# Optimization experiments

Hardware: AMD Instinct MI355X
Metric: run time of the kernel (lower is better)

The kernel has to match this reference:

```python
import jax, jax.numpy as jnp
import numpy as np


def setup_inputs() -> dict:
    key = jax.random.key(0)
    kq, kk, kv = jax.random.split(key, 3)
    d_head, sq, skv = 128, 8192, 8192
    q = jax.random.normal(kq, (d_head, sq), dtype=jnp.float32)
    k = jax.random.normal(kk, (d_head, skv), dtype=jnp.float32)
    v = jax.random.normal(kv, (d_head, skv), dtype=jnp.float32)
    return {"q": q, "k": k, "v": v}


def reference(q, k, v):
    # qk: (seqlen_q, seqlen_kv) -- full score matrix, no 1/sqrt(d) scaling (faithful)
    qk = jnp.einsum('dq,dk->qk', q, k)
    row_max = jnp.max(qk, axis=1, keepdims=True)
    exp_row = jnp.exp(qk - row_max)
    scores = exp_row / jnp.sum(exp_row, axis=1, keepdims=True)
    # attn_out: (seqlen_q, d_head)
    attn_out = jnp.einsum('qk,dk->qd', scores, v)
    return attn_out
```

## Files before the change

kernel.cpp:

```cpp
#include <hip/hip_runtime.h>
#include <hip/hip_bf16.h>
#include <math.h>

typedef _Float16 half8 __attribute__((ext_vector_type(8)));
typedef __fp16 fp16x2 __attribute__((ext_vector_type(2)));
typedef float f32x4 __attribute__((ext_vector_type(4)));
typedef float f32x16 __attribute__((ext_vector_type(16)));

#define D 128
#define SQ 8192
#define SKV 8192
#define BQ 128
#define BKV 64
#define LOG2E 1.4426950408889634f
#define DEFER_THR 11.5417f

__device__ __forceinline__ ushort f2bf(float x) {
  union { float f; unsigned u; } v; v.f = x;
  unsigned r = v.u + 0x7fffu + ((v.u >> 16) & 1u);
  return (ushort)(r >> 16);
}
__device__ __forceinline__ float bf2f(ushort h) {
  union { unsigned u; float f; } v; v.u = ((unsigned)h) << 16;
  return v.f;
}
__device__ __forceinline__ unsigned cvtpk_bf(float a, float b) {
  unsigned r;
  asm("v_cvt_pk_bf16_f32 %0, %1, %2" : "=v"(r) : "v"(a), "v"(b));
  return r;
}
__device__ __forceinline__ unsigned cvtpk_h(float a, float b) {
  union { fp16x2 h; unsigned u; } r;
  r.h = __builtin_amdgcn_cvt_pkrtz(a, b);
  return r.u;
}
__device__ __forceinline__ float fexp2(float x) {
  float r;
  asm("v_exp_f32 %0, %1" : "=v"(r) : "v"(x));
  return r;
}
__device__ __forceinline__ void pl32swap(unsigned& a, unsigned& b) {
  asm("v_permlane32_swap_b32 %0, %1" : "+v"(a), "+v"(b));
}

__global__ void prep_all(const float* __restrict__ q, const float* __restrict__ k,
                         const float* __restrict__ v,
                         _Float16* __restrict__ QT, _Float16* __restrict__ PK,
                         _Float16* __restrict__ PV) {
  int b = blockIdx.x;
  int t = threadIdx.x;
  if (b < 512) {
    const bool isQ = (b < 256);
    const float* src = isQ ? q : k;
    const float scl = isQ ? LOG2E : 1.0f;
    int s0 = (isQ ? b : b - 256) * 32;
    __shared__ float lds[128][33];
    int dr = t >> 5, l = t & 31;
#pragma unroll
    for (int j = 0; j < 16; ++j) {
      int dd = dr * 16 + j;
      lds[dd][l] = src[(size_t)dd * SQ + s0 + l];
    }
    __syncthreads();
#pragma unroll
    for (int i = 0; i < 2; ++i) {
      int cid = t + i * 256;
      int c = cid >> 5, sl = cid & 31;
      half8 hv;
#pragma unroll
      for (int e = 0; e < 8; ++e) hv[e] = (_Float16)(lds[c * 8 + e][sl] * scl);
      if (isQ) {
        *(half8*)(QT + (size_t)(s0 + sl) * D + c * 8) = hv;
      } else {
        int srow = s0 + sl;
        size_t elem = (size_t)((srow >> 5) * 8 + (c >> 1)) * 512 +
                      ((c & 1) * 32 + (srow & 31)) * 8;
        *(half8*)(PK + elem) = hv;
      }
    }
  } else {
    int idx = (b - 512) * 256 + t;
    int i8 = idx * 8;
    float4 x0 = *(const float4*)(v + i8);
    float4 x1 = *(const float4*)(v + i8 + 4);
    int drow = i8 >> 13;
    int kv = i8 & (SKV - 1);
    size_t elem = (size_t)(kv >> 6) * 8192 +
                  (size_t)((drow >> 5) * 4 + ((kv >> 4) & 3)) * 512 +
                  (((kv >> 3) & 1) * 32 + (drow & 31)) * 8;
    half8 hv = { (_Float16)x0.x, (_Float16)x0.y, (_Float16)x0.z, (_Float16)x0.w,
                 (_Float16)x1.x, (_Float16)x1.y, (_Float16)x1.z, (_Float16)x1.w };
    *(half8*)(PV + elem) = hv;
  }
}

__global__ __launch_bounds__(256, 2)
void flash_fwd(const _Float16* __restrict__ QT, const _Float16* __restrict__ PK,
               const _Float16* __restrict__ PV,
               ushort* __restrict__ Opart, float* __restrict__ Mst,
               float* __restrict__ Lst, int splitLen) {
  __shared__ _Float16 Kl[2][BKV * D];
  __shared__ _Float16 Vl[2][BKV * D];

  if (blockIdx.y & 4) __builtin_amdgcn_s_sleep(60);

  const int tid = threadIdx.x;
  const int w = tid >> 6;
  const int lane = tid & 63;
  const int lc = lane & 31;
  const int hi = lane >> 5;
  const int qb = blockIdx.x;
  const int split = blockIdx.y;
  const int qrow = qb * BQ + w * 32 + lc;

  half8 qh[8];
#pragma unroll
  for (int ds = 0; ds < 8; ++ds)
    qh[ds] = *(const half8*)(QT + (size_t)qrow * D + ds * 16 + hi * 8);

  f32x16 Ot[4];
#pragma unroll
  for (int dt = 0; dt < 4; ++dt)
#pragma unroll
    for (int e = 0; e < 16; ++e) Ot[dt][e] = 0.f;
  float mrun = -INFINITY, lrun = 0.f;

  const int kvBase = split * splitLen;
  const int nsteps = splitLen / BKV;

#define STAGE(NB, KV0)                                                        \
  {                                                                           \
    _Pragma("unroll")                                                         \
    for (int j = 0; j < 8; ++j) {                                             \
      int cblk = w * 8 + j;                                                   \
      int cc = cblk & 15;                                                     \
      const _Float16* gp = ((cblk < 16) ? PK : PV) +                          \
                           (size_t)(KV0) * D + cc * 512 + lane * 8;           \
      _Float16* lp = ((cblk < 16) ? &Kl[NB][0] : &Vl[NB][0]) + cc * 512;      \
      __builtin_amdgcn_global_load_lds(                                       \
          (const __attribute__((address_space(1))) unsigned*)gp,              \
          (__attribute__((address_space(3))) unsigned*)lp, 16, 0, 0);         \
    }                                                                         \
  }

  STAGE(0, kvBase);
  __syncthreads();
  int cur = 0;

  for (int it = 0; it < nsteps; ++it) {
    const int kv0 = kvBase + it * BKV;
    const bool more = (it + 1 < nsteps);
    if (more) STAGE(cur ^ 1, kv0 + BKV);

    const _Float16* kb = &Kl[cur][0] + lane * 8;
    const _Float16* vb = &Vl[cur][0] + lane * 8;

    half8 ka[16];
#pragma unroll
    for (int j = 0; j < 16; ++j) ka[j] = *(const half8*)(kb + j * 512);

    f32x16 s0, s1;
#pragma unroll
    for (int e = 0; e < 16; ++e) { s0[e] = 0.f; s1[e] = 0.f; }
    __builtin_amdgcn_s_setprio(1);
#pragma unroll
    for (int ds = 0; ds < 8; ++ds) {
      s0 = __builtin_amdgcn_mfma_f32_32x32x16_f16(ka[ds], qh[ds], s0, 0, 0, 0);
      s1 = __builtin_amdgcn_mfma_f32_32x32x16_f16(ka[8 + ds], qh[ds], s1, 0, 0, 0);
    }
    __builtin_amdgcn_s_setprio(0);

    half8 va[16];
#pragma unroll
    for (int f = 0; f < 16; ++f) va[f] = *(const half8*)(vb + f * 512);

    float t8[8];
#pragma unroll
    for (int e = 0; e < 8; ++e)
      t8[e] = fmaxf(fmaxf(s0[e], s0[e + 8]), fmaxf(s1[e], s1[e + 8]));
    float mx = fmaxf(fmaxf(fmaxf(t8[0], t8[4]), fmaxf(t8[1], t8[5])),
                     fmaxf(fmaxf(t8[2], t8[6]), fmaxf(t8[3], t8[7])));
    mx = fmaxf(mx, __shfl_xor(mx, 32));

    if (!__all(mx - mrun <= DEFER_THR)) {
      float mn = fmaxf(mrun, mx);
      float sc = fexp2(mrun - mn);
      mrun = mn;
      lrun *= sc;
#pragma unroll
      for (int dt = 0; dt < 4; ++dt)
#pragma unroll
        for (int e = 0; e < 16; ++e) Ot[dt][e] *= sc;
    }

#pragma unroll
    for (int e = 0; e < 16; ++e) {
      s0[e] = fexp2(s0[e] - mrun);
      s1[e] = fexp2(s1[e] - mrun);
    }
    float a8[8];
#pragma unroll
    for (int e = 0; e < 8; ++e) a8[e] = (s0[e] + s0[e + 8]) + (s1[e] + s1[e + 8]);
    float lsum = ((a8[0] + a8[4]) + (a8[1] + a8[5])) +
                 ((a8[2] + a8[6]) + (a8[3] + a8[7]));
    lsum += __shfl_xor(lsum, 32);
    lrun += lsum;

    unsigned pk[8];
    half8 pb[4];
    union { unsigned u[4]; half8 v; } pbu;
#pragma unroll
    for (int j = 0; j < 8; ++j) pk[j] = cvtpk_h(s0[2 * j], s0[2 * j + 1]);
    pl32swap(pk[0], pk[2]); pl32swap(pk[1], pk[3]);
    pl32swap(pk[4], pk[6]); pl32swap(pk[5], pk[7]);
    pbu.u[0] = pk[0]; pbu.u[1] = pk[1]; pbu.u[2] = pk[2]; pbu.u[3] = pk[3]; pb[0] = pbu.v;
    pbu.u[0] = pk[4]; pbu.u[1] = pk[5]; pbu.u[2] = pk[6]; pbu.u[3] = pk[7]; pb[1] = pbu.v;
#pragma unroll
    for (int j = 0; j < 8; ++j) pk[j] = cvtpk_h(s1[2 * j], s1[2 * j + 1]);
    pl32swap(pk[0], pk[2]); pl32swap(pk[1], pk[3]);
    pl32swap(pk[4], pk[6]); pl32swap(pk[5], pk[7]);
    pbu.u[0] = pk[0]; pbu.u[1] = pk[1]; pbu.u[2] = pk[2]; pbu.u[3] = pk[3]; pb[2] = pbu.v;
    pbu.u[0] = pk[4]; pbu.u[1] = pk[5]; pbu.u[2] = pk[6]; pbu.u[3] = pk[7]; pb[3] = pbu.v;

    __builtin_amdgcn_s_setprio(1);
#pragma unroll
    for (int cc = 0; cc < 4; ++cc) {
      Ot[0] = __builtin_amdgcn_mfma_f32_32x32x16_f16(va[0 * 4 + cc], pb[cc], Ot[0], 0, 0, 0);
      Ot[1] = __builtin_amdgcn_mfma_f32_32x32x16_f16(va[1 * 4 + cc], pb[cc], Ot[1], 0, 0, 0);
      Ot[2] = __builtin_amdgcn_mfma_f32_32x32x16_f16(va[2 * 4 + cc], pb[cc], Ot[2], 0, 0, 0);
      Ot[3] = __builtin_amdgcn_mfma_f32_32x32x16_f16(va[3 * 4 + cc], pb[cc], Ot[3], 0, 0, 0);
    }
    __builtin_amdgcn_s_setprio(0);

    __syncthreads();
    cur ^= 1;
  }

  ushort* Op = Opart + (size_t)split * SQ * D + (size_t)qrow * D;
#pragma unroll
  for (int dt = 0; dt < 4; ++dt) {
#pragma unroll
    for (int rg = 0; rg < 4; ++rg) {
      uint2 o2;
      o2.x = cvtpk_bf(Ot[dt][4 * rg + 0], Ot[dt][4 * rg + 1]);
      o2.y = cvtpk_bf(Ot[dt][4 * rg + 2], Ot[dt][4 * rg + 3]);
      *(uint2*)(Op + dt * 32 + rg * 8 + hi * 4) = o2;
    }
  }
  if (hi == 0) {
    Mst[split * SQ + qrow] = mrun;
    Lst[split * SQ + qrow] = lrun;
  }
}

__global__ void combine(const ushort* __restrict__ Opart, const float* __restrict__ Mst,
                        const float* __restrict__ Lst, float* __restrict__ out, int nsplit) {
  int t4 = (blockIdx.x * 256 + threadIdx.x) * 4;
  int qi = t4 >> 7;
  float M = -INFINITY;
  for (int s = 0; s < nsplit; ++s) M = fmaxf(M, Mst[s * SQ + qi]);
  float n0 = 0.f, n1 = 0.f, n2 = 0.f, n3 = 0.f, den = 0.f;
  for (int s = 0; s < nsplit; ++s) {
    float wgt = fexp2(Mst[s * SQ + qi] - M);
    den += wgt * Lst[s * SQ + qi];
    ushort4 u = *(const ushort4*)(Opart + (size_t)s * SQ * D + t4);
    n0 += wgt * bf2f(u.x); n1 += wgt * bf2f(u.y);
    n2 += wgt * bf2f(u.z); n3 += wgt * bf2f(u.w);
  }
  float inv = 1.0f / den;
  float4 o = { n0 * inv, n1 * inv, n2 * inv, n3 * inv };
  *(float4*)(out + t4) = o;
}

extern "C" void kernel_launch(void* const* d_in, const int* in_sizes, int n_in,
                              void* d_out, int out_size, void* d_ws, size_t ws_size,
                              hipStream_t stream) {
  const float* q = (const float*)d_in[0];
  const float* k = (const float*)d_in[1];
  const float* v = (const float*)d_in[2];
  float* out = (float*)d_out;

  char* ws = (char*)d_ws;
  const size_t mat = (size_t)SQ * D * 2;
  _Float16* QT = (_Float16*)(ws);
  _Float16* PK = (_Float16*)(ws + mat);
  _Float16* PV = (_Float16*)(ws + 2 * mat);
  char* rest = ws + 3 * mat;

  const size_t opartSz = (size_t)SQ * D * 2;
  const size_t statSz  = (size_t)SQ * 4;
  int nsplit = 8;
  while (nsplit > 1 &&
         3 * mat + (size_t)nsplit * (opartSz + 2 * statSz) > ws_size) nsplit >>= 1;

  ushort* Opart = (ushort*)rest;
  float* Mst = (float*)(rest + (size_t)nsplit * opartSz);
  float* Lst = (float*)(rest + (size_t)nsplit * opartSz + (size_t)nsplit * statSz);

  prep_all<<<1024, 256, 0, stream>>>(q, k, v, QT, PK, PV);
  flash_fwd<<<dim3(SQ / BQ, nsplit), 256, 0, stream>>>(QT, PK, PV,
                                                       Opart, Mst, Lst, SKV / nsplit);
  combine<<<(SQ * D) / (256 * 4), 256, 0, stream>>>(Opart, Mst, Lst, out, nsplit);
}
```

Baseline: 60.31 us.

## Double query tile to 256 rows with 8 waves and per-subtile online softmax

Doubles the query block to 256 rows handled by 8 waves of 512 threads, so each staged K/V tile in LDS serves twice as many query rows and global-to-LDS traffic per query halves. The softmax and PV update now run per 32-column subtile, and half the waves process the two subtiles in reverse order to stagger MFMA and exp phases across waves. The stagger sleep for upper splits is removed. Risks include fewer blocks in the grid, lower occupancy from 512-thread blocks under the same register budget, and more frequent rescale checks per step.

```diff
diff --git a/kernel.cpp b/kernel.cpp
--- a/kernel.cpp
+++ b/kernel.cpp
@@ -10,7 +10,7 @@
 #define D 128
 #define SQ 8192
 #define SKV 8192
-#define BQ 128
+#define BQ 256
 #define BKV 64
 #define LOG2E 1.4426950408889634f
 #define DEFER_THR 11.5417f
@@ -94,15 +94,13 @@
   }
 }
 
-__global__ __launch_bounds__(256, 2)
+__global__ __launch_bounds__(512, 2)
 void flash_fwd(const _Float16* __restrict__ QT, const _Float16* __restrict__ PK,
                const _Float16* __restrict__ PV,
                ushort* __restrict__ Opart, float* __restrict__ Mst,
                float* __restrict__ Lst, int splitLen) {
   __shared__ _Float16 Kl[2][BKV * D];
   __shared__ _Float16 Vl[2][BKV * D];
-
-  if (blockIdx.y & 4) __builtin_amdgcn_s_sleep(60);
 
   const int tid = threadIdx.x;
   const int w = tid >> 6;
@@ -131,8 +129,8 @@
 #define STAGE(NB, KV0)                                                        \
   {                                                                           \
     _Pragma("unroll")                                                         \
-    for (int j = 0; j < 8; ++j) {                                             \
-      int cblk = w * 8 + j;                                                   \
+    for (int j = 0; j < 4; ++j) {                                             \
+      int cblk = w * 4 + j;                                                   \
       int cc = cblk & 15;                                                     \
       const _Float16* gp = ((cblk < 16) ? PK : PV) +                          \
                            (size_t)(KV0) * D + cc * 512 + lane * 8;           \
@@ -147,41 +145,26 @@
   __syncthreads();
   int cur = 0;
 
-  for (int it = 0; it < nsteps; ++it) {
-    const int kv0 = kvBase + it * BKV;
-    const bool more = (it + 1 < nsteps);
-    if (more) STAGE(cur ^ 1, kv0 + BKV);
-
-    const _Float16* kb = &Kl[cur][0] + lane * 8;
-    const _Float16* vb = &Vl[cur][0] + lane * 8;
-
-    half8 ka[16];
-#pragma unroll
-    for (int j = 0; j < 16; ++j) ka[j] = *(const half8*)(kb + j * 512);
-
-    f32x16 s0, s1;
-#pragma unroll
-    for (int e = 0; e < 16; ++e) { s0[e] = 0.f; s1[e] = 0.f; }
+  half8 ka[16];
+  half8 va[16];
+
+  auto qkh = [&](f32x16& s, int off) {
+#pragma unroll
+    for (int e = 0; e < 16; ++e) s[e] = 0.f;
     __builtin_amdgcn_s_setprio(1);
 #pragma unroll
-    for (int ds = 0; ds < 8; ++ds) {
-      s0 = __builtin_amdgcn_mfma_f32_32x32x16_f16(ka[ds], qh[ds], s0, 0, 0, 0);
-      s1 = __builtin_amdgcn_mfma_f32_32x32x16_f16(ka[8 + ds], qh[ds], s1, 0, 0, 0);
-    }
+    for (int ds = 0; ds < 8; ++ds)
+      s = __builtin_amdgcn_mfma_f32_32x32x16_f16(ka[off + ds], qh[ds], s, 0, 0, 0);
     __builtin_amdgcn_s_setprio(0);
-
-    half8 va[16];
-#pragma unroll
-    for (int f = 0; f < 16; ++f) va[f] = *(const half8*)(vb + f * 512);
-
-    float t8[8];
-#pragma unroll
-    for (int e = 0; e < 8; ++e)
-      t8[e] = fmaxf(fmaxf(s0[e], s0[e + 8]), fmaxf(s1[e], s1[e + 8]));
-    float mx = fmaxf(fmaxf(fmaxf(t8[0], t8[4]), fmaxf(t8[1], t8[5])),
-                     fmaxf(fmaxf(t8[2], t8[6]), fmaxf(t8[3], t8[7])));
+  };
+
+  auto subtile = [&](f32x16& s, int cbase) {
+    float t4a = fmaxf(fmaxf(s[0], s[4]), fmaxf(s[8], s[12]));
+    float t4b = fmaxf(fmaxf(s[1], s[5]), fmaxf(s[9], s[13]));
+    float t4c = fmaxf(fmaxf(s[2], s[6]), fmaxf(s[10], s[14]));
+    float t4d = fmaxf(fmaxf(s[3], s[7]), fmaxf(s[11], s[15]));
+    float mx = fmaxf(fmaxf(t4a, t4b), fmaxf(t4c, t4d));
     mx = fmaxf(mx, __shfl_xor(mx, 32));
-
     if (!__all(mx - mrun <= DEFER_THR)) {
       float mn = fmaxf(mrun, mx);
       float sc = fexp2(mrun - mn);
@@ -192,45 +175,61 @@
 #pragma unroll
         for (int e = 0; e < 16; ++e) Ot[dt][e] *= sc;
     }
-
-#pragma unroll
-    for (int e = 0; e < 16; ++e) {
-      s0[e] = fexp2(s0[e] - mrun);
-      s1[e] = fexp2(s1[e] - mrun);
-    }
-    float a8[8];
-#pragma unroll
-    for (int e = 0; e < 8; ++e) a8[e] = (s0[e] + s0[e + 8]) + (s1[e] + s1[e + 8]);
-    float lsum = ((a8[0] + a8[4]) + (a8[1] + a8[5])) +
-                 ((a8[2] + a8[6]) + (a8[3] + a8[7]));
+#pragma unroll
+    for (int e = 0; e < 16; ++e) s[e] = fexp2(s[e] - mrun);
+    float a4a = (s[0] + s[4]) + (s[8] + s[12]);
+    float a4b = (s[1] + s[5]) + (s[9] + s[13]);
+    float a4c = (s[2] + s[6]) + (s[10] + s[14]);
+    float a4d = (s[3] + s[7]) + (s[11] + s[15]);
+    float lsum = (a4a + a4b) + (a4c + a4d);
     lsum += __shfl_xor(lsum, 32);
     lrun += lsum;
 
     unsigned pk[8];
-    half8 pb[4];
+    half8 pb0, pb1;
     union { unsigned u[4]; half8 v; } pbu;
 #pragma unroll
-    for (int j = 0; j < 8; ++j) pk[j] = cvtpk_h(s0[2 * j], s0[2 * j + 1]);
+    for (int j = 0; j < 8; ++j) pk[j] = cvtpk_h(s[2 * j], s[2 * j + 1]);
     pl32swap(pk[0], pk[2]); pl32swap(pk[1], pk[3]);
     pl32swap(pk[4], pk[6]); pl32swap(pk[5], pk[7]);
-    pbu.u[0] = pk[0]; pbu.u[1] = pk[1]; pbu.u[2] = pk[2]; pbu.u[3] = pk[3]; pb[0] = pbu.v;
-    pbu.u[0] = pk[4]; pbu.u[1] = pk[5]; pbu.u[2] = pk[6]; pbu.u[3] = pk[7]; pb[1] = pbu.v;
-#pragma unroll
-    for (int j = 0; j < 8; ++j) pk[j] = cvtpk_h(s1[2 * j], s1[2 * j + 1]);
-    pl32swap(pk[0], pk[2]); pl32swap(pk[1], pk[3]);
-    pl32swap(pk[4], pk[6]); pl32swap(pk[5], pk[7]);
-    pbu.u[0] = pk[0]; pbu.u[1] = pk[1]; pbu.u[2] = pk[2]; pbu.u[3] = pk[3]; pb[2] = pbu.v;
-    pbu.u[0] = pk[4]; pbu.u[1] = pk[5]; pbu.u[2] = pk[6]; pbu.u[3] = pk[7]; pb[3] = pbu.v;
+    pbu.u[0] = pk[0]; pbu.u[1] = pk[1]; pbu.u[2] = pk[2]; pbu.u[3] = pk[3]; pb0 = pbu.v;
+    pbu.u[0] = pk[4]; pbu.u[1] = pk[5]; pbu.u[2] = pk[6]; pbu.u[3] = pk[7]; pb1 = pbu.v;
 
     __builtin_amdgcn_s_setprio(1);
 #pragma unroll
-    for (int cc = 0; cc < 4; ++cc) {
-      Ot[0] = __builtin_amdgcn_mfma_f32_32x32x16_f16(va[0 * 4 + cc], pb[cc], Ot[0], 0, 0, 0);
-      Ot[1] = __builtin_amdgcn_mfma_f32_32x32x16_f16(va[1 * 4 + cc], pb[cc], Ot[1], 0, 0, 0);
-      Ot[2] = __builtin_amdgcn_mfma_f32_32x32x16_f16(va[2 * 4 + cc], pb[cc], Ot[2], 0, 0, 0);
-      Ot[3] = __builtin_amdgcn_mfma_f32_32x32x16_f16(va[3 * 4 + cc], pb[cc], Ot[3], 0, 0, 0);
+    for (int dt = 0; dt < 4; ++dt) {
+      Ot[dt] = __builtin_amdgcn_mfma_f32_32x32x16_f16(va[dt * 4 + cbase], pb0, Ot[dt], 0, 0, 0);
+      Ot[dt] = __builtin_amdgcn_mfma_f32_32x32x16_f16(va[dt * 4 + cbase + 1], pb1, Ot[dt], 0, 0, 0);
     }
     __builtin_amdgcn_s_setprio(0);
+  };
+
+  for (int it = 0; it < nsteps; ++it) {
+    const int kv0 = kvBase + it * BKV;
+    const bool more = (it + 1 < nsteps);
+    if (more) STAGE(cur ^ 1, kv0 + BKV);
+
+    const _Float16* kb = &Kl[cur][0] + lane * 8;
+    const _Float16* vb = &Vl[cur][0] + lane * 8;
+#pragma unroll
+    for (int j = 0; j < 16; ++j) ka[j] = *(const half8*)(kb + j * 512);
+
+    f32x16 s0, s1;
+    if (w < 4) {
+      qkh(s0, 0);
+      qkh(s1, 8);
+#pragma unroll
+      for (int f = 0; f < 16; ++f) va[f] = *(const half8*)(vb + f * 512);
+      subtile(s0, 0);
+      subtile(s1, 2);
+    } else {
+      qkh(s1, 8);
+      qkh(s0, 0);
+#pragma unroll
+      for (int f = 0; f < 16; ++f) va[f] = *(const half8*)(vb + f * 512);
+      subtile(s1, 2);
+      subtile(s0, 0);
+    }
 
     __syncthreads();
     cur ^= 1;
@@ -298,7 +297,7 @@
   float* Lst = (float*)(rest + (size_t)nsplit * opartSz + (size_t)nsplit * statSz);
 
   prep_all<<<1024, 256, 0, stream>>>(q, k, v, QT, PK, PV);
-  flash_fwd<<<dim3(SQ / BQ, nsplit), 256, 0, stream>>>(QT, PK, PV,
+  flash_fwd<<<dim3(SQ / BQ, nsplit), 512, 0, stream>>>(QT, PK, PV,
                                                        Opart, Mst, Lst, SKV / nsplit);
   combine<<<(SQ * D) / (256 * 4), 256, 0, stream>>>(Opart, Mst, Lst, out, nsplit);
 }
```

Result: no change. 61.26 us (+1.6%).

## Software-pipeline QK and softmax-PV across KV tiles with 512-thread blocks

Applied to the files above, without the earlier changes.

Doubles the query tile to 256 rows with 8 waves per block, so each staged K/V tile is shared by twice as many rows. The main loop becomes a two-stage software pipeline: QK^T for tile t+1 is issued alongside softmax and PV for tile t, with V triple-buffered in LDS and K double-buffered. K/V fragments are now read from LDS just before each MFMA instead of being held in large register arrays. The staggered s_sleep for some splits is removed. This targets MFMA idle time and K/V load traffic, at the cost of more LDS, fewer blocks in the grid and higher register pressure from holding two score tiles.

```diff
diff --git a/kernel.cpp b/kernel.cpp
--- a/kernel.cpp
+++ b/kernel.cpp
@@ -10,16 +10,11 @@
 #define D 128
 #define SQ 8192
 #define SKV 8192
-#define BQ 128
+#define BQ 256
 #define BKV 64
 #define LOG2E 1.4426950408889634f
 #define DEFER_THR 11.5417f
 
-__device__ __forceinline__ ushort f2bf(float x) {
-  union { float f; unsigned u; } v; v.f = x;
-  unsigned r = v.u + 0x7fffu + ((v.u >> 16) & 1u);
-  return (ushort)(r >> 16);
-}
 __device__ __forceinline__ float bf2f(ushort h) {
   union { unsigned u; float f; } v; v.u = ((unsigned)h) << 16;
   return v.f;
@@ -94,15 +89,13 @@
   }
 }
 
-__global__ __launch_bounds__(256, 2)
+__global__ __launch_bounds__(512, 2)
 void flash_fwd(const _Float16* __restrict__ QT, const _Float16* __restrict__ PK,
                const _Float16* __restrict__ PV,
                ushort* __restrict__ Opart, float* __restrict__ Mst,
                float* __restrict__ Lst, int splitLen) {
   __shared__ _Float16 Kl[2][BKV * D];
-  __shared__ _Float16 Vl[2][BKV * D];
-
-  if (blockIdx.y & 4) __builtin_amdgcn_s_sleep(60);
+  __shared__ _Float16 Vl[3][BKV * D];
 
   const int tid = threadIdx.x;
   const int w = tid >> 6;
@@ -127,53 +120,39 @@
 
   const int kvBase = split * splitLen;
   const int nsteps = splitLen / BKV;
-
-#define STAGE(NB, KV0)                                                        \
+  const int tB = kvBase / BKV;
+
+#define STAGE(KB, VB, T)                                                      \
   {                                                                           \
     _Pragma("unroll")                                                         \
-    for (int j = 0; j < 8; ++j) {                                             \
-      int cblk = w * 8 + j;                                                   \
+    for (int j = 0; j < 4; ++j) {                                             \
+      int cblk = w * 4 + j;                                                   \
       int cc = cblk & 15;                                                     \
       const _Float16* gp = ((cblk < 16) ? PK : PV) +                          \
-                           (size_t)(KV0) * D + cc * 512 + lane * 8;           \
-      _Float16* lp = ((cblk < 16) ? &Kl[NB][0] : &Vl[NB][0]) + cc * 512;      \
+                           (size_t)(T) * (BKV * D) + cc * 512 + lane * 8;     \
+      _Float16* lp = ((cblk < 16) ? &Kl[KB][0] : &Vl[VB][0]) + cc * 512;      \
       __builtin_amdgcn_global_load_lds(                                       \
           (const __attribute__((address_space(1))) unsigned*)gp,              \
           (__attribute__((address_space(3))) unsigned*)lp, 16, 0, 0);         \
     }                                                                         \
   }
 
-  STAGE(0, kvBase);
-  __syncthreads();
-  int cur = 0;
-
-  for (int it = 0; it < nsteps; ++it) {
-    const int kv0 = kvBase + it * BKV;
-    const bool more = (it + 1 < nsteps);
-    if (more) STAGE(cur ^ 1, kv0 + BKV);
-
-    const _Float16* kb = &Kl[cur][0] + lane * 8;
-    const _Float16* vb = &Vl[cur][0] + lane * 8;
-
-    half8 ka[16];
-#pragma unroll
-    for (int j = 0; j < 16; ++j) ka[j] = *(const half8*)(kb + j * 512);
-
-    f32x16 s0, s1;
+  auto QKX = [&](int kb2, f32x16& s0, f32x16& s1) {
+    const _Float16* kb = &Kl[kb2][0] + lane * 8;
 #pragma unroll
     for (int e = 0; e < 16; ++e) { s0[e] = 0.f; s1[e] = 0.f; }
     __builtin_amdgcn_s_setprio(1);
 #pragma unroll
     for (int ds = 0; ds < 8; ++ds) {
-      s0 = __builtin_amdgcn_mfma_f32_32x32x16_f16(ka[ds], qh[ds], s0, 0, 0, 0);
-      s1 = __builtin_amdgcn_mfma_f32_32x32x16_f16(ka[8 + ds], qh[ds], s1, 0, 0, 0);
+      half8 k0 = *(const half8*)(kb + ds * 512);
+      half8 k1 = *(const half8*)(kb + (8 + ds) * 512);
+      s0 = __builtin_amdgcn_mfma_f32_32x32x16_f16(k0, qh[ds], s0, 0, 0, 0);
+      s1 = __builtin_amdgcn_mfma_f32_32x32x16_f16(k1, qh[ds], s1, 0, 0, 0);
     }
     __builtin_amdgcn_s_setprio(0);
-
-    half8 va[16];
-#pragma unroll
-    for (int f = 0; f < 16; ++f) va[f] = *(const half8*)(vb + f * 512);
-
+  };
+
+  auto SMPV = [&](f32x16& s0, f32x16& s1, int vb3) {
     float t8[8];
 #pragma unroll
     for (int e = 0; e < 8; ++e)
@@ -181,7 +160,6 @@
     float mx = fmaxf(fmaxf(fmaxf(t8[0], t8[4]), fmaxf(t8[1], t8[5])),
                      fmaxf(fmaxf(t8[2], t8[6]), fmaxf(t8[3], t8[7])));
     mx = fmaxf(mx, __shfl_xor(mx, 32));
-
     if (!__all(mx - mrun <= DEFER_THR)) {
       float mn = fmaxf(mrun, mx);
       float sc = fexp2(mrun - mn);
@@ -192,7 +170,6 @@
 #pragma unroll
         for (int e = 0; e < 16; ++e) Ot[dt][e] *= sc;
     }
-
 #pragma unroll
     for (int e = 0; e < 16; ++e) {
       s0[e] = fexp2(s0[e] - mrun);
@@ -222,18 +199,47 @@
     pbu.u[0] = pk[0]; pbu.u[1] = pk[1]; pbu.u[2] = pk[2]; pbu.u[3] = pk[3]; pb[2] = pbu.v;
     pbu.u[0] = pk[4]; pbu.u[1] = pk[5]; pbu.u[2] = pk[6]; pbu.u[3] = pk[7]; pb[3] = pbu.v;
 
+    const _Float16* vb = &Vl[vb3][0] + lane * 8;
     __builtin_amdgcn_s_setprio(1);
 #pragma unroll
-    for (int cc = 0; cc < 4; ++cc) {
-      Ot[0] = __builtin_amdgcn_mfma_f32_32x32x16_f16(va[0 * 4 + cc], pb[cc], Ot[0], 0, 0, 0);
-      Ot[1] = __builtin_amdgcn_mfma_f32_32x32x16_f16(va[1 * 4 + cc], pb[cc], Ot[1], 0, 0, 0);
-      Ot[2] = __builtin_amdgcn_mfma_f32_32x32x16_f16(va[2 * 4 + cc], pb[cc], Ot[2], 0, 0, 0);
-      Ot[3] = __builtin_amdgcn_mfma_f32_32x32x16_f16(va[3 * 4 + cc], pb[cc], Ot[3], 0, 0, 0);
+    for (int dt = 0; dt < 4; ++dt) {
+      half8 v0 = *(const half8*)(vb + (dt * 4 + 0) * 512);
+      half8 v1 = *(const half8*)(vb + (dt * 4 + 1) * 512);
+      half8 v2 = *(const half8*)(vb + (dt * 4 + 2) * 512);
+      half8 v3 = *(const half8*)(vb + (dt * 4 + 3) * 512);
+      Ot[dt] = __builtin_amdgcn_mfma_f32_32x32x16_f16(v0, pb[0], Ot[dt], 0, 0, 0);
+      Ot[dt] = __builtin_amdgcn_mfma_f32_32x32x16_f16(v1, pb[1], Ot[dt], 0, 0, 0);
+      Ot[dt] = __builtin_amdgcn_mfma_f32_32x32x16_f16(v2, pb[2], Ot[dt], 0, 0, 0);
+      Ot[dt] = __builtin_amdgcn_mfma_f32_32x32x16_f16(v3, pb[3], Ot[dt], 0, 0, 0);
     }
     __builtin_amdgcn_s_setprio(0);
-
+  };
+
+  f32x16 sA0, sA1, sB0, sB1;
+
+  STAGE(0, 0, tB);
+  __syncthreads();
+  if (nsteps > 1) STAGE(1, 1, tB + 1);
+  QKX(0, sA0, sA1);
+  __syncthreads();
+
+  int p = 1;
+  for (; p + 1 < nsteps; p += 2) {
+    STAGE(0, (p + 1) % 3, tB + p + 1);
+    QKX(1, sB0, sB1);
+    SMPV(sA0, sA1, (p - 1) % 3);
     __syncthreads();
-    cur ^= 1;
+    if (p + 2 < nsteps) STAGE(1, (p + 2) % 3, tB + p + 2);
+    QKX(0, sA0, sA1);
+    SMPV(sB0, sB1, p % 3);
+    __syncthreads();
+  }
+  if (p < nsteps) {
+    QKX(1, sB0, sB1);
+    SMPV(sA0, sA1, (p - 1) % 3);
+    SMPV(sB0, sB1, p % 3);
+  } else {
+    SMPV(sA0, sA1, (nsteps - 1) % 3);
   }
 
   ushort* Op = Opart + (size_t)split * SQ * D + (size_t)qrow * D;
@@ -298,7 +304,7 @@
   float* Lst = (float*)(rest + (size_t)nsplit * opartSz + (size_t)nsplit * statSz);
 
   prep_all<<<1024, 256, 0, stream>>>(q, k, v, QT, PK, PV);
-  flash_fwd<<<dim3(SQ / BQ, nsplit), 256, 0, stream>>>(QT, PK, PV,
+  flash_fwd<<<dim3(SQ / BQ, nsplit), 512, 0, stream>>>(QT, PK, PV,
                                                        Opart, Mst, Lst, SKV / nsplit);
   combine<<<(SQ * D) / (256 * 4), 256, 0, stream>>>(Opart, Mst, Lst, out, nsplit);
 }
```

Result: faster. 58.51 us (-3.0%).
